# Optimization experiments

Hardware: AMD Instinct MI355X
Metric: run time of the kernel (lower is better)

Reference implementation:

```python
import jax, jax.numpy as jnp
import numpy as np

N = 100000   # nodes
E = 800000   # edges
H = 128      # hidden_dim
HOP = 3
B = 64       # graphs


def setup_inputs() -> dict:
    key = jax.random.key(0)
    ks = jax.random.split(key, 24)
    s = 0.05
    x = jnp.round(jax.random.uniform(ks[0], (N, 1))).astype(jnp.float32)  # binary node indicator
    edge_index = jax.random.randint(ks[1], (2, E), 0, N)
    edge_attr = jax.random.normal(ks[2], (E, 1), dtype=jnp.float32)
    batch = jnp.sort(jax.random.randint(ks[3], (N,), 0, B))
    p = lambda k, sh: (s * jax.random.normal(k, sh)).astype(jnp.float32)
    return dict(
        x=x, edge_index=edge_index, edge_attr=edge_attr, batch=batch, num_graphs=B,
        l0_w=p(ks[4], (HOP, 1, H)), l0_b=p(ks[5], (HOP, H)),
        l1_w=p(ks[6], (HOP, H, H)), l1_b=p(ks[7], (HOP, H)),
        l2_w=p(ks[8], (HOP, 1, H)), l2_b=p(ks[9], (HOP, H)),
        l3_w=p(ks[10], (HOP, 1, 1)), l3_b=p(ks[11], (HOP, 1)),
        att_w=p(ks[12], (2 * H, H)), att_b=p(ks[13], (H,)),
        sp_w=p(ks[14], (H, H)), sp_b=p(ks[15], (H,)),
        ac_w=p(ks[16], (2 * H, H)), ac_b=p(ks[17], (H,)),
        last_w=p(ks[18], (2 * H, 1)), last_b=p(ks[19], (1,)),
    )


def _seg_mean(v, idx, m):
    # scatter-mean into m buckets; empty buckets -> 0 (matches PyG MeanAggregation)
    s = jax.ops.segment_sum(v, idx, num_segments=m)
    c = jax.ops.segment_sum(jnp.ones((v.shape[0], 1), v.dtype), idx, num_segments=m)
    return jnp.where(c > 0, s / jnp.maximum(c, 1.0), 0.0)


def reference(x, edge_index, edge_attr, batch, num_graphs,
              l0_w, l0_b, l1_w, l1_b, l2_w, l2_b, l3_w, l3_b,
              att_w, att_b, sp_w, sp_b, ac_w, ac_b, last_w, last_b):
    n = x.shape[0]
    row, col = edge_index[0], edge_index[1]
    hop, hid = l0_w.shape[0], l0_w.shape[2]
    u = jnp.zeros((n, hid), x.dtype)
    for i in range(hop):
        first = x @ l0_w[i] + l0_b[i]                      # [N,H]
        u_agg = _seg_mean(edge_attr * u[col], row, n)      # gather + scatter-mean
        second = u_agg @ l1_w[i] + l1_b[i]
        ee = jax.nn.relu(edge_attr @ l3_w[i] + l3_b[i])    # [E,1]
        third = _seg_mean(ee, row, n) @ l2_w[i] + l2_b[i]
        u = jax.nn.relu(first + second + third)
    # per-graph cluster embeddings (global_mean_pool ratios)
    h_c_0 = _seg_mean(u * (1 - x), batch, num_graphs) / _seg_mean(1 - x, batch, num_graphs)
    h_c_1 = _seg_mean(u * x, batch, num_graphs) / _seg_mean(x, batch, num_graphs)
    hc0, hc1 = h_c_0[batch], h_c_1[batch]                  # [N,H]
    tce = x * hc0 + (1 - x) * hc1
    h_a = jnp.concatenate([u, tce], axis=-1)               # [N,2H]
    att = h_a @ att_w + att_b
    w0 = jnp.sum(att * hc0, axis=1, keepdims=True)
    w1 = jnp.sum(att * hc1, axis=1, keepdims=True)
    w = jax.nn.softmax(jnp.concatenate([w0, w1], axis=-1), axis=-1)
    h_s = w[:, :1] * hc0 + w[:, 1:] * hc1
    q = jnp.concatenate([h_s @ sp_w + sp_b, h_a @ ac_w + ac_b], axis=-1) @ last_w + last_b
    return q
```

## Files before the change

kernel.cpp:

```cpp
#include <hip/hip_runtime.h>
#include <stdint.h>

typedef unsigned int  u32;
typedef unsigned short u16;

typedef short bf16x8 __attribute__((ext_vector_type(8)));
typedef float f32x4  __attribute__((ext_vector_type(4)));

static __device__ __forceinline__ float b2f(u16 h){
    union { u32 u; float f; } v; v.u = ((u32)h) << 16; return v.f;
}
static __device__ __forceinline__ float b2f_hi(u32 w){
    union { u32 u; float f; } v; v.u = w & 0xFFFF0000u; return v.f;
}
static __device__ __forceinline__ float b2f_lo(u32 w){
    union { u32 u; float f; } v; v.u = w << 16; return v.f;
}
static __device__ __forceinline__ u16 f2b(float f){
    union { float f; u32 u; } v; v.f = f;
    u32 r = v.u + 0x7FFFu + ((v.u >> 16) & 1u);
    return (u16)(r >> 16);
}
static __device__ __forceinline__ u32 cvt_pk(float lo, float hi){
    u32 r; asm("v_cvt_pk_bf16_f32 %0, %1, %2" : "=v"(r) : "v"(lo), "v"(hi));
    return r;
}
static __device__ __forceinline__ u16 f2b1(float f){
    u32 r; asm("v_cvt_pk_bf16_f32 %0, %1, %2" : "=v"(r) : "v"(f), "v"(f));
    return (u16)r;
}

#define OL0W 0
#define OL0B 384
#define OL1W 768
#define OL1B 49920
#define OL2W 50304
#define OL2B 50688
#define OL3W 51072
#define OL3B 51075
#define OATTW 51078
#define OATTB 83846
#define OSPW 83974
#define OSPB 100358
#define OACW 100486
#define OACB 133254
#define OLASTW 133382
#define OLASTB 133638
#define WTOT 133639

#define PREPW_BLOCKS 192
#define ECAP 40

struct Ptrs16 { const void* p[16]; };

static __device__ __forceinline__ int detect_bf(const u32* __restrict__ xw){
    int lane = threadIdx.x & 63;
    int f = 0;
    #pragma unroll
    for (int i = 0; i < 8; ++i){
        u32 w = xw[lane * 8 + i];
        f |= ((w & 0xFFFFu) == 0x3F80u) ? 1 : 0;
    }
    return __ballot(f) != 0ull;
}

__global__ __launch_bounds__(256) void k_prep(Ptrs16 wp, const void* __restrict__ xin,
                                              float* __restrict__ wc, float* __restrict__ xc,
                                              u16* __restrict__ w1t, float* __restrict__ basev,
                                              int* __restrict__ flag,
                                              const int* __restrict__ row, const int* __restrict__ col,
                                              const void* __restrict__ ea,
                                              int* __restrict__ cnt, int2* __restrict__ ecs,
                                              int scatBase, int E, int N){
    int b = blockIdx.x, t = threadIdx.x;
    int bf = detect_bf((const u32*)xin);
    if (b >= scatBase){
        int e0 = ((b - scatBase) * 256 + t) * 4;
        if (e0 >= E) return;
        int rr[4], cc[4]; float av[4];
        if (e0 + 3 < E){
            int4 rv = *(const int4*)(row + e0);
            int4 cv = *(const int4*)(col + e0);
            rr[0]=rv.x; rr[1]=rv.y; rr[2]=rv.z; rr[3]=rv.w;
            cc[0]=cv.x; cc[1]=cv.y; cc[2]=cv.z; cc[3]=cv.w;
            if (bf){
                ushort4 ev = *(const ushort4*)((const u16*)ea + e0);
                av[0]=b2f(ev.x); av[1]=b2f(ev.y); av[2]=b2f(ev.z); av[3]=b2f(ev.w);
            } else {
                float4 ev = *(const float4*)((const float*)ea + e0);
                av[0]=ev.x; av[1]=ev.y; av[2]=ev.z; av[3]=ev.w;
            }
        } else {
            #pragma unroll
            for (int j = 0; j < 4; ++j){
                int e = e0 + j;
                rr[j] = (e < E) ? row[e] : 0;
                cc[j] = (e < E) ? col[e] : 0;
                av[j] = (e < E) ? (bf ? b2f(((const u16*)ea)[e]) : ((const float*)ea)[e]) : 0.f;
            }
        }
        int slot[4];
        #pragma unroll
        for (int j = 0; j < 4; ++j)
            slot[j] = (e0 + j < E) ? atomicAdd(&cnt[rr[j]], 1) : ECAP;
        #pragma unroll
        for (int j = 0; j < 4; ++j)
            if (e0 + j < E && slot[j] < ECAP)
                ecs[(size_t)rr[j] * ECAP + slot[j]] = make_int2(cc[j], __float_as_int(av[j]));
        return;
    }
    auto rd = [&](int seg, int off) -> float {
        return bf ? b2f(((const u16*)wp.p[seg])[off]) : ((const float*)wp.p[seg])[off];
    };
    if (b < PREPW_BLOCKS){
        int id = b * 256 + t;
        int i = id >> 14, rem = id & 16383;
        int n = rem >> 7, k = rem & 127;
        w1t[(i * 128 + n) * 128 + k] = f2b(rd(2, (i * 128 + k) * 128 + n));
        if (id < 384) basev[id] = rd(1, id) + rd(3, id) + rd(5, id);
        if (id == 0) *flag = bf;
    } else {
        int i = (b - PREPW_BLOCKS) * 256 + t;
        const int sz[16] = {384,384,49152,384,384,384,3,3,32768,128,16384,128,32768,128,256,1};
        if (i < WTOT){
            int seg = 0, off = i;
            while (off >= sz[seg]){ off -= sz[seg]; ++seg; }
            wc[i] = rd(seg, off);
        } else {
            int n = i - WTOT;
            if (n < N) xc[n] = bf ? b2f(((const u16*)xin)[n]) : ((const float*)xin)[n];
        }
    }
}

__global__ __launch_bounds__(256) void k_hop0(const int2* __restrict__ ecs, const int* __restrict__ cnt,
                                              const float* __restrict__ xc, const float* __restrict__ wc,
                                              float* __restrict__ t12, const float* __restrict__ basev,
                                              float* __restrict__ spf, float* __restrict__ acf,
                                              float* __restrict__ biasv,
                                              uint4* __restrict__ uOut, int foldBlk, int N){
    if ((int)blockIdx.x == foldBlk){
        int t = threadIdx.x;
        const float* aw  = wc + OACW + t * 128;
        const float* lw2 = wc + OLASTW + 128;
        float s = 0.f;
        #pragma unroll 8
        for (int o = 0; o < 128; ++o) s += aw[o] * lw2[o];
        acf[t] = s;
        if (t < 128){
            const float* sw = wc + OSPW + t * 128;
            const float* lw = wc + OLASTW;
            float s2 = 0.f;
            #pragma unroll 8
            for (int o = 0; o < 128; ++o) s2 += sw[o] * lw[o];
            spf[t] = s2;
        }
        float pb = 0.f;
        if (t < 128) pb = wc[OSPB + t] * wc[OLASTW + t] + wc[OACB + t] * wc[OLASTW + 128 + t];
        __shared__ float red[4];
        #pragma unroll
        for (int m = 1; m < 64; m <<= 1) pb += __shfl_xor(pb, m);
        if ((t & 63) == 0) red[t >> 6] = pb;
        __syncthreads();
        if (t == 0) biasv[0] = red[0] + red[1] + red[2] + red[3] + wc[OLASTB];
        return;
    }
    int id = blockIdx.x * 256 + threadIdx.x;
    int n = id >> 4;
    if (n >= N) return;
    int sl = threadIdx.x & 15;
    float w30 = wc[OL3W + 0], w31 = wc[OL3W + 1], w32 = wc[OL3W + 2];
    float c30 = wc[OL3B + 0], c31 = wc[OL3B + 1], c32 = wc[OL3B + 2];
    int d = min(cnt[n], ECAP);
    size_t s = (size_t)n * ECAP;
    float s0 = 0.f, s1 = 0.f, s2 = 0.f;
    for (int e = sl; e < d; e += 16){
        float a = __int_as_float(ecs[s + e].y);
        s0 += fmaxf(a * w30 + c30, 0.f);
        s1 += fmaxf(a * w31 + c31, 0.f);
        s2 += fmaxf(a * w32 + c32, 0.f);
    }
    #pragma unroll
    for (int m = 1; m < 16; m <<= 1){
        s0 += __shfl_xor(s0, m);
        s1 += __shfl_xor(s1, m);
        s2 += __shfl_xor(s2, m);
    }
    float iv = d > 0 ? 1.0f / (float)d : 0.f;
    if (sl == 0){ t12[n] = s1 * iv; t12[N + n] = s2 * iv; }
    float t0 = s0 * iv;
    float xv = xc[n];
    int j = sl * 8;
    const float* l0wc = wc + OL0W;
    const float* l2wc = wc + OL2W;
    u32 w[4];
    #pragma unroll
    for (int k = 0; k < 4; ++k){
        float va = fmaxf(xv * l0wc[j + 2*k]     + t0 * l2wc[j + 2*k]     + basev[j + 2*k],     0.f);
        float vb = fmaxf(xv * l0wc[j + 2*k + 1] + t0 * l2wc[j + 2*k + 1] + basev[j + 2*k + 1], 0.f);
        w[k] = cvt_pk(va, vb);
    }
    uOut[id] = make_uint4(w[0], w[1], w[2], w[3]);
}

#define ACC8(acc, g, p) \
    acc[0] += g * b2f_lo(p.x); acc[1] += g * b2f_hi(p.x); \
    acc[2] += g * b2f_lo(p.y); acc[3] += g * b2f_hi(p.y); \
    acc[4] += g * b2f_lo(p.z); acc[5] += g * b2f_hi(p.z); \
    acc[6] += g * b2f_lo(p.w); acc[7] += g * b2f_hi(p.w);

template<int POOL>
__global__ __launch_bounds__(256) void k_hop(const u16* __restrict__ uPrev, u16* __restrict__ uNext,
    const int2* __restrict__ ecs, const int* __restrict__ cnt,
    const u16* __restrict__ w1t, const float* __restrict__ basev,
    const float* __restrict__ l0wc, const float* __restrict__ l2wc,
    const float* __restrict__ xc, const float* __restrict__ t_i,
    const int* __restrict__ batch, float* __restrict__ S0, float* __restrict__ S1,
    int* __restrict__ cnt1, int N)
{
    __shared__ __align__(16) u16 A[32][136];
    __shared__ __align__(8) int2 esh[32][17];
    __shared__ int dsh[32];
    int tid = threadIdx.x;
    int lane = tid & 63, wid = tid >> 6;
    int n0 = blockIdx.x * 32;
    int cid = lane & 15, grp = lane >> 4;

    {
        int sr = tid >> 3, sl = tid & 7;
        int sn = n0 + sr;
        if (sn < N){
            size_t sb = (size_t)sn * ECAP;
            esh[sr][sl]     = ecs[sb + sl];
            esh[sr][sl + 8] = ecs[sb + sl + 8];
            if (sl == 0) dsh[sr] = min(cnt[sn], ECAP);
        }
    }

    #pragma unroll
    for (int p = 0; p < 2; ++p){
        int r = wid * 8 + p * 4 + grp;
        int n = n0 + r;
        float acc[8];
        #pragma unroll
        for (int j = 0; j < 8; ++j) acc[j] = 0.f;
        if (n < N){
            int d = dsh[r];
            int m = min(d, 16);
            for (int e = 0; e < m; e += 4){
                int i1 = (e + 1 < m) ? e + 1 : 0;
                int i2 = (e + 2 < m) ? e + 2 : 0;
                int i3 = (e + 3 < m) ? e + 3 : 0;
                int2 m0 = esh[r][e], m1 = esh[r][i1], m2 = esh[r][i2], m3 = esh[r][i3];
                float g0 = __int_as_float(m0.y);
                float g1 = (e + 1 < m) ? __int_as_float(m1.y) : 0.f;
                float g2 = (e + 2 < m) ? __int_as_float(m2.y) : 0.f;
                float g3 = (e + 3 < m) ? __int_as_float(m3.y) : 0.f;
                uint4 p0 = *(const uint4*)(uPrev + (size_t)m0.x * 128 + cid * 8);
                uint4 p1 = *(const uint4*)(uPrev + (size_t)m1.x * 128 + cid * 8);
                uint4 p2 = *(const uint4*)(uPrev + (size_t)m2.x * 128 + cid * 8);
                uint4 p3 = *(const uint4*)(uPrev + (size_t)m3.x * 128 + cid * 8);
                ACC8(acc, g0, p0); ACC8(acc, g1, p1);
                ACC8(acc, g2, p2); ACC8(acc, g3, p3);
            }
            size_t s = (size_t)n * ECAP;
            for (int e = 16; e < d; ++e){
                int2 mm = ecs[s + e];
                float g = __int_as_float(mm.y);
                uint4 pp = *(const uint4*)(uPrev + (size_t)mm.x * 128 + cid * 8);
                ACC8(acc, g, pp);
            }
            float sc = d > 0 ? 1.0f / (float)d : 0.f;
            uint4 o;
            o.x = cvt_pk(acc[0] * sc, acc[1] * sc);
            o.y = cvt_pk(acc[2] * sc, acc[3] * sc);
            o.z = cvt_pk(acc[4] * sc, acc[5] * sc);
            o.w = cvt_pk(acc[6] * sc, acc[7] * sc);
            *(uint4*)&A[r][cid * 8] = o;
        } else {
            *(uint4*)&A[r][cid * 8] = make_uint4(0u, 0u, 0u, 0u);
        }
    }
    __syncthreads();

    bf16x8 bfr[4][2];
    #pragma unroll
    for (int kk = 0; kk < 4; ++kk)
        #pragma unroll
        for (int nt = 0; nt < 2; ++nt)
            bfr[kk][nt] = *(const bf16x8*)(w1t + (size_t)(wid * 32 + nt * 16 + cid) * 128 + kk * 32 + grp * 8);

    f32x4 acc4[2][2];
    #pragma unroll
    for (int mt = 0; mt < 2; ++mt)
        #pragma unroll
        for (int nt = 0; nt < 2; ++nt) acc4[mt][nt] = (f32x4){0.f, 0.f, 0.f, 0.f};
    #pragma unroll
    for (int kk = 0; kk < 4; ++kk){
        int kb = kk * 32 + grp * 8;
        bf16x8 af[2];
        #pragma unroll
        for (int mt = 0; mt < 2; ++mt) af[mt] = *(const bf16x8*)&A[mt * 16 + cid][kb];
        #pragma unroll
        for (int mt = 0; mt < 2; ++mt)
            #pragma unroll
            for (int nt = 0; nt < 2; ++nt)
                acc4[mt][nt] = __builtin_amdgcn_mfma_f32_16x16x32_bf16(af[mt], bfr[kk][nt], acc4[mt][nt], 0, 0, 0);
    }

    float w0c[2], w2c[2], bc[2]; int colv[2];
    #pragma unroll
    for (int nt = 0; nt < 2; ++nt){
        int col = wid * 32 + nt * 16 + cid;
        colv[nt] = col;
        w0c[nt] = l0wc[col]; w2c[nt] = l2wc[col]; bc[nt] = basev[col];
    }
    int gLo = 0, gHi = 0;
    float accP[8];
    if (POOL){
        gLo = batch[n0];
        gHi = batch[min(n0 + 31, N - 1)];
        #pragma unroll
        for (int j = 0; j < 8; ++j) accP[j] = 0.f;
    }
    #pragma unroll
    for (int mt = 0; mt < 2; ++mt){
        #pragma unroll
        for (int rg = 0; rg < 4; ++rg){
            int n = n0 + mt * 16 + grp * 4 + rg;
            if (n < N){
                float xv = xc[n];
                float tv = t_i[n];
                int sel = 0;
                if (POOL){
                    sel = ((batch[n] != gLo) ? 2 : 0) + ((xv > 0.5f) ? 1 : 0);
                }
                #pragma unroll
                for (int nt = 0; nt < 2; ++nt){
                    float v = fmaxf(acc4[mt][nt][rg] + xv * w0c[nt] + tv * w2c[nt] + bc[nt], 0.f);
                    uNext[(size_t)n * 128 + colv[nt]] = f2b1(v);
                    if (POOL) accP[nt * 4 + sel] += v;
                }
            }
        }
    }
    if (POOL){
        #pragma unroll
        for (int j = 0; j < 8; ++j){
            accP[j] += __shfl_xor(accP[j], 16);
            accP[j] += __shfl_xor(accP[j], 32);
        }
        if (grp == 0){
            #pragma unroll
            for (int nt = 0; nt < 2; ++nt){
                atomicAdd(&S0[gLo * 128 + colv[nt]], accP[nt * 4 + 0]);
                atomicAdd(&S1[gLo * 128 + colv[nt]], accP[nt * 4 + 1]);
                if (gHi != gLo){
                    atomicAdd(&S0[gHi * 128 + colv[nt]], accP[nt * 4 + 2]);
                    atomicAdd(&S1[gHi * 128 + colv[nt]], accP[nt * 4 + 3]);
                }
            }
        }
        if (wid == 0){
            int n = n0 + lane;
            int ok = (lane < 32 && n < N) ? 1 : 0;
            int is1 = ok && (xc[n] > 0.5f);
            int hi  = ok && (batch[n] != gLo);
            unsigned long long mLo = __ballot(is1 && !hi);
            unsigned long long mHi = __ballot(is1 && hi);
            if (lane == 0){
                int c = __popcll(mLo);
                if (c) atomicAdd(&cnt1[gLo], c);
                c = __popcll(mHi);
                if (c && gHi != gLo) atomicAdd(&cnt1[gHi], c);
            }
        }
    }
}


static __device__ __forceinline__ int lowbound(const int* b, int n, int g){
    int lo = 0, hi = n;
    while (lo < hi){ int m = (lo + hi) >> 1; if (b[m] < g) lo = m + 1; else hi = m; }
    return lo;
}

__global__ __launch_bounds__(256) void k_graph(const float* __restrict__ S0, const float* __restrict__ S1,
                                               const int* __restrict__ cnt1, const int* __restrict__ batch,
                                               const float* __restrict__ wc, const float* __restrict__ spf,
                                               const float* __restrict__ acf,
                                               float* __restrict__ v0, float* __restrict__ v1,
                                               float* __restrict__ gsc, int N){
    __shared__ float h0[128], h1[128], sv0[128], sv1[128];
    int g = blockIdx.x, t = threadIdx.x;
    int st = lowbound(batch, N, g), en = lowbound(batch, N, g + 1);
    int c1 = cnt1[g], c0 = (en - st) - c1;
    if (t < 128){
        h0[t] = c0 > 0 ? S0[g * 128 + t] / (float)c0 : 0.f;
        h1[t] = c1 > 0 ? S1[g * 128 + t] / (float)c1 : 0.f;
    }
    __syncthreads();
    float a0 = 0.f, a1 = 0.f;
    for (int o = 0; o < 128; ++o){
        float w = wc[OATTW + t * 128 + o];
        a0 += w * h0[o];
        a1 += w * h1[o];
    }
    v0[g * 256 + t] = a0; v1[g * 256 + t] = a1;
    if (t >= 128){ sv0[t - 128] = a0; sv1[t - 128] = a1; }
    __syncthreads();
    if (t < 64){
        int l = t;
        float p[10];
        #pragma unroll
        for (int k = 0; k < 10; ++k) p[k] = 0.f;
        #pragma unroll
        for (int rep = 0; rep < 2; ++rep){
            int o = l + rep * 64;
            float hh0 = h0[o], hh1 = h1[o];
            float q0 = sv0[o], q1 = sv1[o];
            float ab = wc[OATTB + o];
            float sf = spf[o], af = acf[128 + o];
            p[0] += q0 * hh0; p[1] += q0 * hh1;
            p[2] += q1 * hh0; p[3] += q1 * hh1;
            p[4] += ab * hh0; p[5] += ab * hh1;
            p[6] += sf * hh0; p[7] += sf * hh1;
            p[8] += af * hh0; p[9] += af * hh1;
        }
        #pragma unroll
        for (int m = 1; m < 64; m <<= 1){
            #pragma unroll
            for (int k = 0; k < 10; ++k) p[k] += __shfl_xor(p[k], m);
        }
        if (l == 0){
            #pragma unroll
            for (int k = 0; k < 10; ++k) gsc[g * 10 + k] = p[k];
        }
    }
}

__global__ __launch_bounds__(256) void k_final(const u16* __restrict__ u, const float* __restrict__ xc,
                                               const int* __restrict__ batch,
                                               const float* __restrict__ v0, const float* __restrict__ v1,
                                               const float* __restrict__ acf, const float* __restrict__ gsc,
                                               const float* __restrict__ biasv, const int* __restrict__ flag,
                                               void* __restrict__ out, int N){
    int bf = *flag;
    int lane = threadIdx.x & 63, wid = threadIdx.x >> 6;
    int sub = lane >> 4, cid = lane & 15;
    int n = blockIdx.x * 16 + wid * 4 + sub;
    if (n >= N) return;
    int g = batch[n];
    int ch = cid * 8;
    uint4 uv = *(const uint4*)(u + (size_t)n * 128 + ch);
    const float* pv0 = v0 + g * 256 + ch;
    const float* pv1 = v1 + g * 256 + ch;
    const float* pac = acf + ch;
    float uu[8] = {b2f_lo(uv.x), b2f_hi(uv.x), b2f_lo(uv.y), b2f_hi(uv.y),
                   b2f_lo(uv.z), b2f_hi(uv.z), b2f_lo(uv.w), b2f_hi(uv.w)};
    float r0 = 0.f, r1 = 0.f, rA = 0.f;
    #pragma unroll
    for (int j = 0; j < 8; ++j){ r0 += uu[j] * pv0[j]; r1 += uu[j] * pv1[j]; rA += uu[j] * pac[j]; }
    #pragma unroll
    for (int m = 1; m < 16; m <<= 1){
        r0 += __shfl_xor(r0, m);
        r1 += __shfl_xor(r1, m);
        rA += __shfl_xor(rA, m);
    }
    if (cid == 0){
        const float* G = gsc + g * 10;
        bool xv = xc[n] > 0.5f;
        float z0 = r0 + (xv ? G[0] : G[1]) + G[4];
        float z1 = r1 + (xv ? G[2] : G[3]) + G[5];
        float mz = fmaxf(z0, z1);
        float e0 = expf(z0 - mz), e1 = expf(z1 - mz);
        float inv = 1.f / (e0 + e1);
        float q = (e0 * G[6] + e1 * G[7]) * inv + rA + (xv ? G[8] : G[9]) + biasv[0];
        if (bf) ((u16*)out)[n] = f2b(q);
        else    ((float*)out)[n] = q;
    }
}


extern "C" void kernel_launch(void* const* d_in, const int* in_sizes, int n_in,
                              void* d_out, int out_size, void* d_ws, size_t ws_size,
                              hipStream_t stream)
{
    const void* x    = d_in[0];
    const int* ei    = (const int*)d_in[1];
    const void* ea   = d_in[2];
    const int* batch = (const int*)d_in[3];
    Ptrs16 wp;
    for (int i = 0; i < 16; ++i) wp.p[i] = d_in[5 + i];

    int N = in_sizes[0];
    int E = in_sizes[2];
    const int* rowI = ei;
    const int* colI = ei + E;

    char* w = (char*)d_ws;
    size_t o = 0;
    auto alloc = [&](size_t b) -> char* {
        char* p = w + o; o = (o + b + 255) & ~(size_t)255; return p;
    };
    int*   flag   = (int*)alloc(4);
    float* basev  = (float*)alloc(3 * 128 * 4);
    float* spf    = (float*)alloc(128 * 4);
    float* acf    = (float*)alloc(256 * 4);
    float* biasv  = (float*)alloc(4);
    float* gsc    = (float*)alloc(64 * 10 * 4);
    float* v0     = (float*)alloc(64 * 256 * 4);
    float* v1     = (float*)alloc(64 * 256 * 4);
    float* wc     = (float*)alloc((size_t)WTOT * 4);
    float* xc     = (float*)alloc((size_t)N * 4);
    float* t12    = (float*)alloc((size_t)2 * N * 4);
    u16*   w1t    = (u16*)alloc((size_t)3 * 128 * 128 * 2);
    u16*   uA     = (u16*)alloc((size_t)N * 128 * 2);
    u16*   uB     = (u16*)alloc((size_t)N * 128 * 2);
    int2*  ecs    = (int2*)alloc((size_t)N * ECAP * 8);
    int*   cnt    = (int*)alloc((size_t)N * 4);
    float* S0     = (float*)alloc(64 * 128 * 4);
    float* S1     = (float*)alloc(64 * 128 * 4);
    int*   cnt1   = (int*)alloc(64 * 4);
    (void)ws_size; (void)n_in; (void)out_size;

    hipMemsetAsync(cnt, 0, (size_t)((char*)cnt1 - (char*)cnt) + 64 * 4, stream);

    int gE4 = (E / 4 + 255) / 256 + 1;
    int canonB = (WTOT + N + 255) / 256;
    int scatBase = PREPW_BLOCKS + canonB;

    k_prep<<<scatBase + gE4, 256, 0, stream>>>(wp, x, wc, xc, w1t, basev, flag,
                                               rowI, colI, ea, cnt, ecs, scatBase, E, N);
    int gHop0 = (N * 16 + 255) / 256;
    k_hop0<<<gHop0 + 1, 256, 0, stream>>>(ecs, cnt, xc, wc, t12, basev, spf, acf, biasv,
                                          (uint4*)uA, gHop0, N);

    int gHop = (N + 31) / 32;
    k_hop<0><<<gHop, 256, 0, stream>>>(uA, uB, ecs, cnt,
                                       w1t + 1 * 16384, basev + 128, wc + OL0W + 128, wc + OL2W + 128,
                                       xc, t12, batch, S0, S1, cnt1, N);
    k_hop<1><<<gHop, 256, 0, stream>>>(uB, uA, ecs, cnt,
                                       w1t + 2 * 16384, basev + 256, wc + OL0W + 256, wc + OL2W + 256,
                                       xc, t12 + N, batch, S0, S1, cnt1, N);

    k_graph<<<64, 256, 0, stream>>>(S0, S1, cnt1, batch, wc, spf, acf, v0, v1, gsc, N);
    k_final<<<(N + 15) / 16, 256, 0, stream>>>(uA, xc, batch, v0, v1, acf, gsc, biasv, flag, d_out, N);
}
```

Baseline: 295.0 us.

## Stage neighbor-row gathers through LDS with direct global-to-LDS loads

The per-edge gather of neighbor feature rows in the hop kernel now issues up to eight 16-byte global_load_lds transfers per wave, writing straight into a per-wave LDS buffer, and then accumulates from LDS. Edges 8-15 are handled in a second batch, and edges beyond 16 keep the old direct-load path. The goal is more loads in flight per wave and fewer VGPRs tied up holding gathered rows. In exchange it adds a 32 KB LDS buffer per block, which can lower occupancy, and explicit vmcnt/lgkmcnt waits that serialize each batch.

```diff
diff --git a/kernel.cpp b/kernel.cpp
--- a/kernel.cpp
+++ b/kernel.cpp
@@ -28,6 +28,11 @@
 static __device__ __forceinline__ u16 f2b1(float f){
     u32 r; asm("v_cvt_pk_bf16_f32 %0, %1, %2" : "=v"(r) : "v"(f), "v"(f));
     return (u16)r;
+}
+
+static __device__ __forceinline__ void gload_lds16(const u16* g, u16* l){
+    __builtin_amdgcn_global_load_lds((const __attribute__((address_space(1))) void*)g,
+                                     (__attribute__((address_space(3))) void*)l, 16, 0, 0);
 }
 
 #define OL0W 0
@@ -219,12 +224,16 @@
     int* __restrict__ cnt1, int N)
 {
     __shared__ __align__(16) u16 A[32][136];
+    __shared__ __align__(16) u16 ubuf[4][8][512];
     __shared__ __align__(8) int2 esh[32][17];
     __shared__ int dsh[32];
     int tid = threadIdx.x;
     int lane = tid & 63, wid = tid >> 6;
     int n0 = blockIdx.x * 32;
     int cid = lane & 15, grp = lane >> 4;
+    int coff = cid * 8;
+    u16* ubw = &ubuf[wid][0][0];
+    u16* ubl = ubw + lane * 8;
 
     {
         int sr = tid >> 3, sl = tid & 7;
@@ -241,33 +250,55 @@
     for (int p = 0; p < 2; ++p){
         int r = wid * 8 + p * 4 + grp;
         int n = n0 + r;
+        int d = 0, m = 0;
+        if (n < N){ d = dsh[r]; m = min(d, 16); }
         float acc[8];
         #pragma unroll
         for (int j = 0; j < 8; ++j) acc[j] = 0.f;
+
+        #pragma unroll
+        for (int e = 0; e < 8; ++e){
+            if (__any(m > e)){
+                int idx = (e < m) ? esh[r][e].x : 0;
+                gload_lds16(uPrev + (size_t)idx * 128 + coff, ubl + e * 512);
+            }
+        }
+        asm volatile("s_waitcnt vmcnt(0)" ::: "memory");
+        __builtin_amdgcn_sched_barrier(0);
+        int mh = min(m, 8);
+        for (int e = 0; e < mh; ++e){
+            int2 me = esh[r][e];
+            float g = __int_as_float(me.y);
+            uint4 pv = *(const uint4*)(ubw + e * 512 + lane * 8);
+            ACC8(acc, g, pv);
+        }
+
+        if (__any(m > 8)){
+            asm volatile("s_waitcnt lgkmcnt(0)" ::: "memory");
+            __builtin_amdgcn_sched_barrier(0);
+            #pragma unroll
+            for (int e = 8; e < 16; ++e){
+                if (__any(m > e)){
+                    int idx = (e < m) ? esh[r][e].x : 0;
+                    gload_lds16(uPrev + (size_t)idx * 128 + coff, ubl + (e - 8) * 512);
+                }
+            }
+            asm volatile("s_waitcnt vmcnt(0)" ::: "memory");
+            __builtin_amdgcn_sched_barrier(0);
+            for (int e = 8; e < m; ++e){
+                int2 me = esh[r][e];
+                float g = __int_as_float(me.y);
+                uint4 pv = *(const uint4*)(ubw + (e - 8) * 512 + lane * 8);
+                ACC8(acc, g, pv);
+            }
+        }
+
         if (n < N){
-            int d = dsh[r];
-            int m = min(d, 16);
-            for (int e = 0; e < m; e += 4){
-                int i1 = (e + 1 < m) ? e + 1 : 0;
-                int i2 = (e + 2 < m) ? e + 2 : 0;
-                int i3 = (e + 3 < m) ? e + 3 : 0;
-                int2 m0 = esh[r][e], m1 = esh[r][i1], m2 = esh[r][i2], m3 = esh[r][i3];
-                float g0 = __int_as_float(m0.y);
-                float g1 = (e + 1 < m) ? __int_as_float(m1.y) : 0.f;
-                float g2 = (e + 2 < m) ? __int_as_float(m2.y) : 0.f;
-                float g3 = (e + 3 < m) ? __int_as_float(m3.y) : 0.f;
-                uint4 p0 = *(const uint4*)(uPrev + (size_t)m0.x * 128 + cid * 8);
-                uint4 p1 = *(const uint4*)(uPrev + (size_t)m1.x * 128 + cid * 8);
-                uint4 p2 = *(const uint4*)(uPrev + (size_t)m2.x * 128 + cid * 8);
-                uint4 p3 = *(const uint4*)(uPrev + (size_t)m3.x * 128 + cid * 8);
-                ACC8(acc, g0, p0); ACC8(acc, g1, p1);
-                ACC8(acc, g2, p2); ACC8(acc, g3, p3);
-            }
             size_t s = (size_t)n * ECAP;
             for (int e = 16; e < d; ++e){
                 int2 mm = ecs[s + e];
                 float g = __int_as_float(mm.y);
-                uint4 pp = *(const uint4*)(uPrev + (size_t)mm.x * 128 + cid * 8);
+                uint4 pp = *(const uint4*)(uPrev + (size_t)mm.x * 128 + coff);
                 ACC8(acc, g, pp);
             }
             float sc = d > 0 ? 1.0f / (float)d : 0.f;
@@ -280,6 +311,8 @@
         } else {
             *(uint4*)&A[r][cid * 8] = make_uint4(0u, 0u, 0u, 0u);
         }
+        asm volatile("s_waitcnt lgkmcnt(0)" ::: "memory");
+        __builtin_amdgcn_sched_barrier(0);
     }
     __syncthreads();
 
```

New measurement: 312.9 us. 6.1% more time.
